# Kernel tuning notes

Hardware: AMD Instinct MI355X
Metric: run time of the kernel (lower is better)

## Reference

```python
import jax, jax.numpy as jnp
import numpy as np

B, S, D, L = 2, 1024, 1024, 48
K = max(1, int(L * 0.1))  # = 4, matches torch k = max(1, int(num_paths * 0.1))
EPS = 1e-5  # torch LayerNorm default


def setup_inputs() -> dict:
    key = jax.random.key(0)
    ks = jax.random.split(key, 7)
    inv = 1.0 / np.sqrt(D).astype(np.float32)
    return {
        "x": jax.random.normal(ks[0], (B, S, D), jnp.float32),
        "gate_w": jax.random.normal(ks[1], (L, D), jnp.float32) * inv,          # gate_proj weight [L,D], no bias
        "lattice_weights": jax.random.normal(ks[2], (L, D, D), jnp.float32) * 0.02,
        "out_w": jax.random.normal(ks[3], (D, D), jnp.float32) * inv,            # out_proj weight [D,D]
        "out_b": jnp.zeros((D,), jnp.float32),
        "ln_g": jnp.ones((D,), jnp.float32),
        "ln_b": jnp.zeros((D,), jnp.float32),
    }


def reference(x, gate_w, lattice_weights, out_w, out_b, ln_g, ln_b):
    # Gate: top-k routing over L lattice paths
    logits = jnp.einsum('bsd,ld->bsl', x, gate_w)                 # [B,S,L]
    top_vals, idx = jax.lax.top_k(logits, K)                      # [B,S,K] each (descending, like torch.topk)
    scores = jax.nn.softmax(top_vals, axis=-1)                    # [B,S,K]

    # Mathematically identical to gathering [B,S,K,D,D] expert matrices and
    # weight-summing, but computed as one dense GEMM over all L experts
    # followed by a cheap gather -- avoids the 32GB intermediate.
    out_all = jnp.einsum('bsd,lde->bsle', x, lattice_weights)     # [B,S,L,D]
    sel = jnp.take_along_axis(out_all, idx[..., None], axis=2)    # [B,S,K,D]
    lattice_out = jnp.einsum('bskd,bsk->bsd', sel, scores)        # [B,S,D]

    y = x + jnp.einsum('bsd,ed->bse', lattice_out, out_w) + out_b # residual + out_proj
    mu = jnp.mean(y, axis=-1, keepdims=True)
    var = jnp.mean((y - mu) ** 2, axis=-1, keepdims=True)
    return ln_g * (y - mu) * jax.lax.rsqrt(var + EPS) + ln_b
```

## Files before the change

### kernel.cpp

```cpp
#include <hip/hip_runtime.h>
#include <stdint.h>

#define TT 2048
#define DD 1024
#define LL 48
#define SENT (LL * 256)

typedef __attribute__((ext_vector_type(8))) short short8;
typedef __attribute__((ext_vector_type(4))) float f32x4;

static __device__ __forceinline__ unsigned int f2bf(float f) {
  union { float f; unsigned int u; } v; v.f = f;
  return (v.u + 0x7FFFu + ((v.u >> 16) & 1u)) >> 16;
}
static __device__ __forceinline__ unsigned int pack2(float a, float b) {
  return f2bf(a) | (f2bf(b) << 16);
}

typedef __attribute__((address_space(1))) const void* as1_t;
typedef __attribute__((address_space(3))) void* as3_t;
static __device__ __forceinline__ void gll16(const void* g, void* s) {
  __builtin_amdgcn_global_load_lds((as1_t)g, (as3_t)s, 16, 0, 0);
}

#define VM_WAIT(n) do { asm volatile("s_waitcnt vmcnt(" #n ")" ::: "memory"); \
                        __builtin_amdgcn_sched_barrier(0); } while (0)
#define LGKM0 do { asm volatile("s_waitcnt lgkmcnt(0)" ::: "memory"); \
                   __builtin_amdgcn_sched_barrier(0); } while (0)
#define BAR do { __builtin_amdgcn_s_barrier(); __builtin_amdgcn_sched_barrier(0); } while (0)

__global__ __launch_bounds__(256) void k_gate(
    const float* __restrict__ x, const float* __restrict__ gw,
    unsigned short* __restrict__ xg, int* __restrict__ counts,
    float* __restrict__ bscore, int* __restrict__ tpos)
{
  __shared__ float xs[8][1024];
  __shared__ float lg[8][48];
  __shared__ int tp_s[32];
  const int tid = threadIdx.x;
  const int t0 = blockIdx.x * 8;
  for (int u = tid; u < 2048; u += 256) {
    int tok = u >> 8;
    int c = (u & 255) << 2;
    float4 v = *(const float4*)(x + (size_t)(t0 + tok) * DD + c);
    *(float4*)&xs[tok][c] = v;
  }
  __syncthreads();
  const int lane = tid & 63, wid = tid >> 6;
  for (int li = 0; li < 12; ++li) {
    const int l = wid + (li << 2);
    const float4* gp = (const float4*)(gw + (size_t)l * DD);
    float4 g0 = gp[lane], g1 = gp[lane + 64], g2 = gp[lane + 128], g3 = gp[lane + 192];
    for (int tok = 0; tok < 8; ++tok) {
      const float4* xp = (const float4*)&xs[tok][0];
      float4 a0 = xp[lane], a1 = xp[lane + 64], a2 = xp[lane + 128], a3 = xp[lane + 192];
      float s = a0.x*g0.x + a0.y*g0.y + a0.z*g0.z + a0.w*g0.w
              + a1.x*g1.x + a1.y*g1.y + a1.z*g1.z + a1.w*g1.w
              + a2.x*g2.x + a2.y*g2.y + a2.z*g2.z + a2.w*g2.w
              + a3.x*g3.x + a3.y*g3.y + a3.z*g3.z + a3.w*g3.w;
      #pragma unroll
      for (int off = 32; off; off >>= 1) s += __shfl_down(s, off);
      if (lane == 0) lg[tok][l] = s;
    }
  }
  __syncthreads();
  if (tid < 8) {
    const int tok = tid;
    float v[4]; int id[4];
    unsigned long long taken = 0ull;
    for (int k = 0; k < 4; ++k) {
      float best = -3.4e38f; int bi = 0;
      for (int l = 0; l < 48; ++l) {
        float cand = lg[tok][l];
        if (!((taken >> l) & 1ull) && cand > best) { best = cand; bi = l; }
      }
      taken |= (1ull << bi); v[k] = best; id[k] = bi;
    }
    float e1 = expf(v[1] - v[0]);
    float e2 = expf(v[2] - v[0]);
    float e3 = expf(v[3] - v[0]);
    float inv = 1.0f / (1.0f + e1 + e2 + e3);
    float sc[4] = { inv, e1*inv, e2*inv, e3*inv };
    for (int k = 0; k < 4; ++k) {
      int pos = atomicAdd(&counts[id[k]], 1);
      bscore[id[k] * TT + pos] = sc[k];
      int dst = (pos < 256) ? (id[k] * 256 + pos) : SENT;
      tp_s[tok * 4 + k] = dst;
      tpos[((t0 + tok) << 2) | k] = dst;
    }
  }
  __syncthreads();
  for (int g = 0; g < 32; ++g) {
    int dst = tp_s[g];
    if (dst == SENT) continue;
    const float* src = xs[g >> 2];
    float a0 = src[tid * 4], a1 = src[tid * 4 + 1], a2 = src[tid * 4 + 2], a3 = src[tid * 4 + 3];
    uint2 pk; pk.x = pack2(a0, a1); pk.y = pack2(a2, a3);
    *(uint2*)(xg + (size_t)dst * DD + tid * 4) = pk;
  }
}

__global__ __launch_bounds__(512, 1) void k_expert(
    const unsigned short* __restrict__ xg, const float* __restrict__ W,
    const int* __restrict__ counts, const float* __restrict__ bscore,
    float* __restrict__ selp)
{
  const int l = blockIdx.y;
  const int ncnt = min(counts[l], 256);
  const int n0 = blockIdx.x * 128;
  const int tid = threadIdx.x, lane = tid & 63, wid = tid >> 6;
  const int wr = wid & 3, wc = wid >> 2;
  const int fr = lane & 15, fq = lane >> 4;

  __shared__ alignas(16) unsigned short As[3][256 * 32];
  __shared__ alignas(16) unsigned int   Bs[2][16 * 132];
  __shared__ float scs[256];
  if (tid < 256) scs[tid] = (tid < ncnt) ? bscore[l * TT + tid] : 0.f;

  const unsigned short* asrc0 = xg + ((size_t)l << 18) + (size_t)(tid >> 2) * DD + (tid & 3) * 8;
  const unsigned short* asrc1 = asrc0 + (size_t)128 * DD;
  const int bp = tid >> 5, e0 = (tid & 31) << 2;
  const float* wsrc0 = W + (size_t)l * DD * DD + (size_t)(bp << 1) * DD + n0 + e0;
  const float* wsrc1 = wsrc0 + DD;

  f32x4 acc[4][4];
  #pragma unroll
  for (int m = 0; m < 4; ++m)
    #pragma unroll
    for (int n = 0; n < 4; ++n)
      #pragma unroll
      for (int j = 0; j < 4; ++j) acc[m][n][j] = 0.f;

  float4 rw0[3], rw1[3];

#define E_BLOAD(s, k0) do { \
    rw0[s] = *(const float4*)(wsrc0 + (size_t)(k0) * DD); \
    rw1[s] = *(const float4*)(wsrc1 + (size_t)(k0) * DD); } while (0)
#define E_ASTAGE(buf, k0) do { \
    gll16(asrc0 + (k0), &As[buf][tid * 8]); \
    gll16(asrc1 + (k0), &As[buf][(512 + tid) * 8]); } while (0)
#define E_BSTORE(buf, s) do { \
    uint4 pv; \
    pv.x = pack2(rw0[s].x, rw1[s].x); pv.y = pack2(rw0[s].y, rw1[s].y); \
    pv.z = pack2(rw0[s].z, rw1[s].z); pv.w = pack2(rw0[s].w, rw1[s].w); \
    *(uint4*)&Bs[buf][bp * 132 + e0] = pv; } while (0)
#define E_COMPUTE(ab, bb) do { \
    const unsigned short* Ab = As[ab]; const unsigned int* Bb = Bs[bb]; \
    short8 af[4], bf[4]; \
    _Pragma("unroll") for (int m = 0; m < 4; ++m) \
      af[m] = *(const short8*)(Ab + (wr * 64 + m * 16 + fr) * 32 + fq * 8); \
    _Pragma("unroll") for (int n = 0; n < 4; ++n) { \
      const int e = wc * 64 + n * 16 + fr; \
      uint4 q; \
      q.x = Bb[(fq * 4 + 0) * 132 + e]; q.y = Bb[(fq * 4 + 1) * 132 + e]; \
      q.z = Bb[(fq * 4 + 2) * 132 + e]; q.w = Bb[(fq * 4 + 3) * 132 + e]; \
      bf[n] = *(short8*)&q; } \
    _Pragma("unroll") for (int m = 0; m < 4; ++m) \
      _Pragma("unroll") for (int n = 0; n < 4; ++n) \
        acc[m][n] = __builtin_amdgcn_mfma_f32_16x16x32_bf16(af[m], bf[n], acc[m][n], 0, 0, 0); \
  } while (0)

  E_BLOAD(0, 0); E_BLOAD(1, 32); E_BLOAD(2, 64);
  E_ASTAGE(0, 0); E_ASTAGE(1, 32);
  VM_WAIT(8);
  E_BSTORE(0, 0);
  E_BLOAD(0, 96);
  VM_WAIT(4);
  LGKM0; BAR;
  E_ASTAGE(2, 64);
  E_COMPUTE(0, 0);
  E_BSTORE(1, 1);
  #pragma unroll
  for (int t = 1; t <= 28; ++t) {
    E_BLOAD((t + 3) % 3, (t + 3) * 32);
    VM_WAIT(6);
    LGKM0; BAR;
    E_ASTAGE((t + 2) % 3, (t + 2) * 32);
    E_COMPUTE(t % 3, t & 1);
    E_BSTORE((t + 1) & 1, (t + 1) % 3);
  }
  VM_WAIT(4);
  LGKM0; BAR;
  E_ASTAGE(1, 31 * 32);
  E_COMPUTE(2, 1);
  E_BSTORE(0, 0);
  VM_WAIT(0);
  LGKM0; BAR;
  E_COMPUTE(0, 0);
  E_BSTORE(1, 1);
  LGKM0; BAR;
  E_COMPUTE(1, 1);

#undef E_BLOAD
#undef E_ASTAGE
#undef E_BSTORE
#undef E_COMPUTE

  #pragma unroll
  for (int m = 0; m < 4; ++m) {
    #pragma unroll
    for (int j = 0; j < 4; ++j) {
      const int r = wr * 64 + m * 16 + fq * 4 + j;
      if (r < ncnt) {
        const float sc = scs[r];
        float* op = selp + (size_t)(l * 256 + r) * DD + n0 + wc * 64 + fr;
        #pragma unroll
        for (int n = 0; n < 4; ++n) op[n * 16] = acc[m][n][j] * sc;
      }
    }
  }
}

__global__ __launch_bounds__(256) void k_combine(const float* __restrict__ selp,
    const int* __restrict__ tpos, unsigned short* __restrict__ lat)
{
  const size_t i = ((size_t)blockIdx.x * 256 + threadIdx.x) << 2;
  const size_t t = i >> 10, d = i & 1023;
  int4 tp = *(const int4*)(tpos + (t << 2));
  float4 s0 = *(const float4*)(selp + (size_t)tp.x * DD + d);
  float4 s1 = *(const float4*)(selp + (size_t)tp.y * DD + d);
  float4 s2 = *(const float4*)(selp + (size_t)tp.z * DD + d);
  float4 s3 = *(const float4*)(selp + (size_t)tp.w * DD + d);
  float r0 = s0.x + s1.x + s2.x + s3.x;
  float r1 = s0.y + s1.y + s2.y + s3.y;
  float r2 = s0.z + s1.z + s2.z + s3.z;
  float r3 = s0.w + s1.w + s2.w + s3.w;
  uint2 pk; pk.x = pack2(r0, r1); pk.y = pack2(r2, r3);
  *(uint2*)(lat + i) = pk;
}

__global__ __launch_bounds__(256, 2) void k_outproj(
    const unsigned short* __restrict__ lat, const float* __restrict__ W2,
    const float* __restrict__ xres, const float* __restrict__ bias,
    float* __restrict__ y)
{
  const int n0 = blockIdx.x * 64;
  const int m0 = blockIdx.y * 128;
  const int tid = threadIdx.x, lane = tid & 63, wid = tid >> 6;

  __shared__ alignas(16) unsigned short As[2][128][40];
  __shared__ alignas(16) unsigned short Bs[2][64][40];

  const int aq = tid >> 2, aseg = tid & 3;
  const unsigned short* la0 = lat + (size_t)(m0 + aq) * DD + aseg * 8;
  const unsigned short* la1 = lat + (size_t)(m0 + aq + 64) * DD + aseg * 8;
  const int be = tid >> 2, bks = tid & 3;
  const float* wb = W2 + (size_t)(n0 + be) * DD + bks * 8;

  f32x4 acc[2][4];
  #pragma unroll
  for (int m = 0; m < 2; ++m)
    #pragma unroll
    for (int n = 0; n < 4; ++n)
      #pragma unroll
      for (int j = 0; j < 4; ++j) acc[m][n][j] = 0.f;

  int4 av0, av1;
  float4 w0, w1;

#define O_LOAD(kk) do { \
    av0 = *(const int4*)(la0 + (kk)); \
    av1 = *(const int4*)(la1 + (kk)); \
    w0 = *(const float4*)(wb + (kk)); \
    w1 = *(const float4*)(wb + (kk) + 4); \
  } while (0)

#define O_STORE(b) do { \
    *(int4*)&As[b][aq][aseg * 8]      = av0; \
    *(int4*)&As[b][aq + 64][aseg * 8] = av1; \
    uint4 pv; \
    pv.x = pack2(w0.x, w0.y); pv.y = pack2(w0.z, w0.w); \
    pv.z = pack2(w1.x, w1.y); pv.w = pack2(w1.z, w1.w); \
    *(uint4*)&Bs[b][be][bks * 8] = pv; \
  } while (0)

  O_LOAD(0); O_STORE(0); __syncthreads();
  int cur = 0;
  for (int t = 0; t < 32; ++t) {
    const bool more = (t < 31);
    if (more) O_LOAD((t + 1) * 32);
    short8 af[2], bf[4];
    #pragma unroll
    for (int n = 0; n < 4; ++n)
      bf[n] = *(const short8*)&Bs[cur][n * 16 + (lane & 15)][(lane >> 4) * 8];
    #pragma unroll
    for (int m = 0; m < 2; ++m)
      af[m] = *(const short8*)&As[cur][wid * 32 + m * 16 + (lane & 15)][(lane >> 4) * 8];
    #pragma unroll
    for (int m = 0; m < 2; ++m)
      #pragma unroll
      for (int n = 0; n < 4; ++n)
        acc[m][n] = __builtin_amdgcn_mfma_f32_16x16x32_bf16(af[m], bf[n], acc[m][n], 0, 0, 0);
    if (more) O_STORE(cur ^ 1);
    __syncthreads();
    cur ^= 1;
  }
#undef O_LOAD
#undef O_STORE

  #pragma unroll
  for (int m = 0; m < 2; ++m) {
    #pragma unroll
    for (int j = 0; j < 4; ++j) {
      const int t = m0 + wid * 32 + m * 16 + ((lane >> 4) << 2) + j;
      #pragma unroll
      for (int n = 0; n < 4; ++n) {
        const int e = n0 + n * 16 + (lane & 15);
        y[(size_t)t * DD + e] = xres[(size_t)t * DD + e] + acc[m][n][j] + bias[e];
      }
    }
  }
}

__global__ __launch_bounds__(256) void k_ln(const float* __restrict__ y,
    const float* __restrict__ g, const float* __restrict__ b, float* __restrict__ out)
{
  const int t = blockIdx.x, tid = threadIdx.x;
  float4 v = *(const float4*)(y + (size_t)t * DD + tid * 4);
  float s  = v.x + v.y + v.z + v.w;
  float ss = v.x*v.x + v.y*v.y + v.z*v.z + v.w*v.w;
  #pragma unroll
  for (int off = 32; off; off >>= 1) { s += __shfl_down(s, off); ss += __shfl_down(ss, off); }
  __shared__ float rs[8];
  const int wid = tid >> 6, lane = tid & 63;
  if (lane == 0) { rs[wid] = s; rs[wid + 4] = ss; }
  __syncthreads();
  float S  = rs[0] + rs[1] + rs[2] + rs[3];
  float SS = rs[4] + rs[5] + rs[6] + rs[7];
  float mu = S * (1.0f / DD);
  float var = SS * (1.0f / DD) - mu * mu;
  float inv = rsqrtf(var + 1e-5f);
  float4 gg = *(const float4*)(g + tid * 4);
  float4 bb = *(const float4*)(b + tid * 4);
  float4 o;
  o.x = gg.x * (v.x - mu) * inv + bb.x;
  o.y = gg.y * (v.y - mu) * inv + bb.y;
  o.z = gg.z * (v.z - mu) * inv + bb.z;
  o.w = gg.w * (v.w - mu) * inv + bb.w;
  *(float4*)(out + (size_t)t * DD + tid * 4) = o;
}

extern "C" void kernel_launch(void* const* d_in, const int* in_sizes, int n_in,
                              void* d_out, int out_size, void* d_ws, size_t ws_size,
                              hipStream_t stream) {
  (void)in_sizes; (void)n_in; (void)out_size;
  const float* x   = (const float*)d_in[0];
  const float* gw  = (const float*)d_in[1];
  const float* lw  = (const float*)d_in[2];
  const float* ow  = (const float*)d_in[3];
  const float* obv = (const float*)d_in[4];
  const float* lng = (const float*)d_in[5];
  const float* lnb = (const float*)d_in[6];
  float* out = (float*)d_out;
  char* ws = (char*)d_ws;

  unsigned short* xg     = (unsigned short*)(ws);
  float*          selp   = (float*)(ws + (24ull << 20));
  unsigned short* lat    = (unsigned short*)(ws + (73ull << 20));
  float*          y      = (float*)(ws + (77ull << 20));
  int*            counts = (int*)(ws + (85ull << 20));
  float*          bscore = (float*)(ws + (85ull << 20) + 4096);
  int*            tpos   = (int*)(ws + (86ull << 20));
  if (ws_size < (87ull << 20)) return;

  hipMemsetAsync(counts, 0, LL * sizeof(int), stream);
  hipMemsetAsync(selp + (size_t)SENT * DD, 0, DD * sizeof(float), stream);
  k_gate<<<TT / 8, 256, 0, stream>>>(x, gw, xg, counts, bscore, tpos);
  k_expert<<<dim3(8, LL), 512, 0, stream>>>(xg, lw, counts, bscore, selp);
  k_combine<<<TT * DD / (256 * 4), 256, 0, stream>>>(selp, tpos, lat);
  k_outproj<<<dim3(16, 16), 256, 0, stream>>>(lat, ow, x, obv, y);
  k_ln<<<TT, 256, 0, stream>>>(y, lng, lnb, out);
}
```

Measured before the change: 193.2 us.

## Shrink expert tile to 256x64, load A fragments directly into registers

The expert GEMM kernel now uses 256-thread blocks covering 64 output columns, giving 768 blocks instead of 384 and allowing up to 3 blocks per CU. The A-operand (gathered bf16 tokens) is no longer staged through LDS with global_load_lds. Each wave reads its MFMA fragments straight from global memory into a double-buffered register set. Only the converted W tile goes through LDS, and the pipeline is restructured around this. The aim is higher occupancy and less LDS traffic, at the cost of uncoalesced 16-byte A reads and more register pressure. Each token row is also reread by every column block, which doubles A global traffic.

Measured after the change: 191.1 us. About the same (-1.1%).

```diff
diff --git a/kernel.cpp b/kernel.cpp
--- a/kernel.cpp
+++ b/kernel.cpp
@@ -17,14 +17,6 @@
   return f2bf(a) | (f2bf(b) << 16);
 }
 
-typedef __attribute__((address_space(1))) const void* as1_t;
-typedef __attribute__((address_space(3))) void* as3_t;
-static __device__ __forceinline__ void gll16(const void* g, void* s) {
-  __builtin_amdgcn_global_load_lds((as1_t)g, (as3_t)s, 16, 0, 0);
-}
-
-#define VM_WAIT(n) do { asm volatile("s_waitcnt vmcnt(" #n ")" ::: "memory"); \
-                        __builtin_amdgcn_sched_barrier(0); } while (0)
 #define LGKM0 do { asm volatile("s_waitcnt lgkmcnt(0)" ::: "memory"); \
                    __builtin_amdgcn_sched_barrier(0); } while (0)
 #define BAR do { __builtin_amdgcn_s_barrier(); __builtin_amdgcn_sched_barrier(0); } while (0)
@@ -100,26 +92,26 @@
   }
 }
 
-__global__ __launch_bounds__(512, 1) void k_expert(
+__global__ __launch_bounds__(256, 3) void k_expert(
     const unsigned short* __restrict__ xg, const float* __restrict__ W,
     const int* __restrict__ counts, const float* __restrict__ bscore,
     float* __restrict__ selp)
 {
   const int l = blockIdx.y;
   const int ncnt = min(counts[l], 256);
-  const int n0 = blockIdx.x * 128;
-  const int tid = threadIdx.x, lane = tid & 63, wid = tid >> 6;
-  const int wr = wid & 3, wc = wid >> 2;
+  const int n0 = blockIdx.x * 64;
+  const int tid = threadIdx.x, lane = tid & 63, wr = tid >> 6;
   const int fr = lane & 15, fq = lane >> 4;
 
-  __shared__ alignas(16) unsigned short As[3][256 * 32];
-  __shared__ alignas(16) unsigned int   Bs[2][16 * 132];
+  __shared__ alignas(16) unsigned int Bs[2][16 * 66];
   __shared__ float scs[256];
-  if (tid < 256) scs[tid] = (tid < ncnt) ? bscore[l * TT + tid] : 0.f;
-
-  const unsigned short* asrc0 = xg + ((size_t)l << 18) + (size_t)(tid >> 2) * DD + (tid & 3) * 8;
-  const unsigned short* asrc1 = asrc0 + (size_t)128 * DD;
-  const int bp = tid >> 5, e0 = (tid & 31) << 2;
+  scs[tid] = (tid < ncnt) ? bscore[l * TT + tid] : 0.f;
+
+  const unsigned short* ap[4];
+  #pragma unroll
+  for (int m = 0; m < 4; ++m)
+    ap[m] = xg + ((size_t)l << 18) + (size_t)(wr * 64 + m * 16 + fr) * DD + fq * 8;
+  const int bp = tid >> 4, e0 = (tid & 15) << 2;
   const float* wsrc0 = W + (size_t)l * DD * DD + (size_t)(bp << 1) * DD + n0 + e0;
   const float* wsrc1 = wsrc0 + DD;
 
@@ -131,70 +123,69 @@
       #pragma unroll
       for (int j = 0; j < 4; ++j) acc[m][n][j] = 0.f;
 
-  float4 rw0[3], rw1[3];
+  short8 af[2][4];
+  float4 rw0[4], rw1[4];
 
 #define E_BLOAD(s, k0) do { \
     rw0[s] = *(const float4*)(wsrc0 + (size_t)(k0) * DD); \
     rw1[s] = *(const float4*)(wsrc1 + (size_t)(k0) * DD); } while (0)
-#define E_ASTAGE(buf, k0) do { \
-    gll16(asrc0 + (k0), &As[buf][tid * 8]); \
-    gll16(asrc1 + (k0), &As[buf][(512 + tid) * 8]); } while (0)
+#define E_ALOAD(p, k0) do { \
+    af[p][0] = *(const short8*)(ap[0] + (k0)); \
+    af[p][1] = *(const short8*)(ap[1] + (k0)); \
+    af[p][2] = *(const short8*)(ap[2] + (k0)); \
+    af[p][3] = *(const short8*)(ap[3] + (k0)); } while (0)
 #define E_BSTORE(buf, s) do { \
     uint4 pv; \
     pv.x = pack2(rw0[s].x, rw1[s].x); pv.y = pack2(rw0[s].y, rw1[s].y); \
     pv.z = pack2(rw0[s].z, rw1[s].z); pv.w = pack2(rw0[s].w, rw1[s].w); \
-    *(uint4*)&Bs[buf][bp * 132 + e0] = pv; } while (0)
-#define E_COMPUTE(ab, bb) do { \
-    const unsigned short* Ab = As[ab]; const unsigned int* Bb = Bs[bb]; \
-    short8 af[4], bf[4]; \
-    _Pragma("unroll") for (int m = 0; m < 4; ++m) \
-      af[m] = *(const short8*)(Ab + (wr * 64 + m * 16 + fr) * 32 + fq * 8); \
+    *(uint4*)&Bs[buf][bp * 66 + e0] = pv; } while (0)
+#define E_COMPUTE(p) do { \
+    const unsigned int* Bb = Bs[p]; \
+    short8 bf[4]; \
     _Pragma("unroll") for (int n = 0; n < 4; ++n) { \
-      const int e = wc * 64 + n * 16 + fr; \
+      const int e = n * 16 + fr; \
       uint4 q; \
-      q.x = Bb[(fq * 4 + 0) * 132 + e]; q.y = Bb[(fq * 4 + 1) * 132 + e]; \
-      q.z = Bb[(fq * 4 + 2) * 132 + e]; q.w = Bb[(fq * 4 + 3) * 132 + e]; \
+      q.x = Bb[(fq * 4 + 0) * 66 + e]; q.y = Bb[(fq * 4 + 1) * 66 + e]; \
+      q.z = Bb[(fq * 4 + 2) * 66 + e]; q.w = Bb[(fq * 4 + 3) * 66 + e]; \
       bf[n] = *(short8*)&q; } \
     _Pragma("unroll") for (int m = 0; m < 4; ++m) \
       _Pragma("unroll") for (int n = 0; n < 4; ++n) \
-        acc[m][n] = __builtin_amdgcn_mfma_f32_16x16x32_bf16(af[m], bf[n], acc[m][n], 0, 0, 0); \
+        acc[m][n] = __builtin_amdgcn_mfma_f32_16x16x32_bf16(af[p][m], bf[n], acc[m][n], 0, 0, 0); \
   } while (0)
 
+#define E_BODY(P, PA, SL, SS, T) do { \
+    E_BLOAD(SL, (T + 3) * 32); \
+    E_ALOAD(PA, (T + 1) * 32); \
+    LGKM0; BAR; \
+    E_BSTORE(PA, SS); \
+    E_COMPUTE(P); } while (0)
+
   E_BLOAD(0, 0); E_BLOAD(1, 32); E_BLOAD(2, 64);
-  E_ASTAGE(0, 0); E_ASTAGE(1, 32);
-  VM_WAIT(8);
+  E_ALOAD(0, 0);
   E_BSTORE(0, 0);
-  E_BLOAD(0, 96);
-  VM_WAIT(4);
+  for (int t = 0; t < 28; t += 4) {
+    E_BODY(0, 1, 3, 1, t + 0);
+    E_BODY(1, 0, 0, 2, t + 1);
+    E_BODY(0, 1, 1, 3, t + 2);
+    E_BODY(1, 0, 2, 0, t + 3);
+  }
+  E_BODY(0, 1, 3, 1, 28);
+  E_ALOAD(0, 30 * 32);
   LGKM0; BAR;
-  E_ASTAGE(2, 64);
-  E_COMPUTE(0, 0);
-  E_BSTORE(1, 1);
-  #pragma unroll
-  for (int t = 1; t <= 28; ++t) {
-    E_BLOAD((t + 3) % 3, (t + 3) * 32);
-    VM_WAIT(6);
-    LGKM0; BAR;
-    E_ASTAGE((t + 2) % 3, (t + 2) * 32);
-    E_COMPUTE(t % 3, t & 1);
-    E_BSTORE((t + 1) & 1, (t + 1) % 3);
-  }
-  VM_WAIT(4);
+  E_BSTORE(0, 2);
+  E_COMPUTE(1);
+  E_ALOAD(1, 31 * 32);
   LGKM0; BAR;
-  E_ASTAGE(1, 31 * 32);
-  E_COMPUTE(2, 1);
-  E_BSTORE(0, 0);
-  VM_WAIT(0);
+  E_BSTORE(1, 3);
+  E_COMPUTE(0);
   LGKM0; BAR;
-  E_COMPUTE(0, 0);
-  E_BSTORE(1, 1);
-  LGKM0; BAR;
-  E_COMPUTE(1, 1);
+  E_COMPUTE(1);
 
 #undef E_BLOAD
-#undef E_ASTAGE
+#undef E_ALOAD
 #undef E_BSTORE
 #undef E_COMPUTE
+#undef E_BODY
 
   #pragma unroll
   for (int m = 0; m < 4; ++m) {
@@ -203,7 +194,7 @@
       const int r = wr * 64 + m * 16 + fq * 4 + j;
       if (r < ncnt) {
         const float sc = scs[r];
-        float* op = selp + (size_t)(l * 256 + r) * DD + n0 + wc * 64 + fr;
+        float* op = selp + (size_t)(l * 256 + r) * DD + n0 + fr;
         #pragma unroll
         for (int n = 0; n < 4; ++n) op[n * 16] = acc[m][n][j] * sc;
       }
@@ -366,7 +357,7 @@
   hipMemsetAsync(counts, 0, LL * sizeof(int), stream);
   hipMemsetAsync(selp + (size_t)SENT * DD, 0, DD * sizeof(float), stream);
   k_gate<<<TT / 8, 256, 0, stream>>>(x, gw, xg, counts, bscore, tpos);
-  k_expert<<<dim3(8, LL), 512, 0, stream>>>(xg, lw, counts, bscore, selp);
+  k_expert<<<dim3(16, LL), 256, 0, stream>>>(xg, lw, counts, bscore, selp);
   k_combine<<<TT * DD / (256 * 4), 256, 0, stream>>>(selp, tpos, lat);
   k_outproj<<<dim3(16, 16), 256, 0, stream>>>(lat, ow, x, obv, y);
   k_ln<<<TT, 256, 0, stream>>>(y, lng, lnb, out);
```

## Pre-convert expert weights to swizzled bf16 and retile expert GEMM

Applied to the files above, without the earlier changes.

Adds a kernel that converts the fp32 expert weights into transposed, XOR-swizzled bf16 each call. The expert GEMM can then stage both A and B straight into LDS with global_load_lds. The GEMM is retiled to 256x256 output tiles with a K step of 64, double buffering and a flat 192-block grid, and gate now writes xg in the matching swizzled layout. This removes the in-register fp32-to-bf16 packing and the bank-conflicted B reads from the GEMM main loop. In exchange it adds an extra pass that reads 192MB of fp32 and writes 96MB of bf16 per call, and needs a larger workspace.

Result: slower. 249.3 us (+29.0%).

```diff
diff --git a/kernel.cpp b/kernel.cpp
--- a/kernel.cpp
+++ b/kernel.cpp
@@ -23,11 +23,11 @@
   __builtin_amdgcn_global_load_lds((as1_t)g, (as3_t)s, 16, 0, 0);
 }
 
-#define VM_WAIT(n) do { asm volatile("s_waitcnt vmcnt(" #n ")" ::: "memory"); \
-                        __builtin_amdgcn_sched_barrier(0); } while (0)
 #define LGKM0 do { asm volatile("s_waitcnt lgkmcnt(0)" ::: "memory"); \
                    __builtin_amdgcn_sched_barrier(0); } while (0)
-#define BAR do { __builtin_amdgcn_s_barrier(); __builtin_amdgcn_sched_barrier(0); } while (0)
+#define VM0   do { asm volatile("s_waitcnt vmcnt(0)" ::: "memory"); \
+                   __builtin_amdgcn_sched_barrier(0); } while (0)
+#define BAR   do { __builtin_amdgcn_s_barrier(); __builtin_amdgcn_sched_barrier(0); } while (0)
 
 __global__ __launch_bounds__(256) void k_gate(
     const float* __restrict__ x, const float* __restrict__ gw,
@@ -90,122 +90,153 @@
     }
   }
   __syncthreads();
-  for (int g = 0; g < 32; ++g) {
-    int dst = tp_s[g];
-    if (dst == SENT) continue;
-    const float* src = xs[g >> 2];
-    float a0 = src[tid * 4], a1 = src[tid * 4 + 1], a2 = src[tid * 4 + 2], a3 = src[tid * 4 + 3];
-    uint2 pk; pk.x = pack2(a0, a1); pk.y = pack2(a2, a3);
-    *(uint2*)(xg + (size_t)dst * DD + tid * 4) = pk;
+  {
+    const int c = tid >> 4, v = (tid >> 1) & 7, h = tid & 1;
+    for (int g = 0; g < 32; ++g) {
+      int dst = tp_s[g];
+      if (dst == SENT) continue;
+      const float* src = xs[g >> 2];
+      float a0 = src[tid*4], a1 = src[tid*4+1], a2 = src[tid*4+2], a3 = src[tid*4+3];
+      uint2 pk; pk.x = pack2(a0, a1); pk.y = pack2(a2, a3);
+      const int p = v ^ (dst & 7);
+      *(uint2*)(xg + (size_t)dst * DD + c * 64 + p * 8 + h * 4) = pk;
+    }
+  }
+}
+
+__global__ __launch_bounds__(256) void k_wconv(const float* __restrict__ W,
+                                               unsigned short* __restrict__ Wt)
+{
+  const int l = blockIdx.z, d0 = blockIdx.y * 128, e0 = blockIdx.x * 128;
+  __shared__ unsigned short T[128][136];
+  const float* src = W + (size_t)l * DD * DD;
+  const int tid = threadIdx.x;
+  #pragma unroll
+  for (int i = 0; i < 16; ++i) {
+    int fl = i * 256 + tid;
+    int d = fl >> 5, e4 = fl & 31;
+    float4 v = *(const float4*)(src + (size_t)(d0 + d) * DD + e0 + e4 * 4);
+    #pragma unroll
+    for (int j = 0; j < 4; ++j) {
+      int e = e4 * 4 + j;
+      int unit = (d >> 3) ^ (e & 7);
+      float fv = (j == 0) ? v.x : (j == 1) ? v.y : (j == 2) ? v.z : v.w;
+      T[e][unit * 8 + (d & 7)] = (unsigned short)f2bf(fv);
+    }
+  }
+  __syncthreads();
+  #pragma unroll
+  for (int i2 = 0; i2 < 8; ++i2) {
+    int uo = i2 * 256 + tid;
+    int e = uo >> 4, ds = uo & 15;
+    short8 s8 = *(const short8*)&T[e][(ds ^ (e & 7)) * 8];
+    int od = d0 + (ds >> 3) * 64 + (((ds & 7) ^ (e & 7)) * 8);
+    *(short8*)(Wt + ((size_t)l << 20) + (size_t)(e0 + e) * DD + od) = s8;
   }
 }
 
 __global__ __launch_bounds__(512, 1) void k_expert(
-    const unsigned short* __restrict__ xg, const float* __restrict__ W,
+    const unsigned short* __restrict__ xg, const unsigned short* __restrict__ Wt,
     const int* __restrict__ counts, const float* __restrict__ bscore,
     float* __restrict__ selp)
 {
-  const int l = blockIdx.y;
+  const int bid = blockIdx.x;
+  const int l = bid % LL;
+  const int n0 = (bid / LL) * 256;
   const int ncnt = min(counts[l], 256);
-  const int n0 = blockIdx.x * 128;
   const int tid = threadIdx.x, lane = tid & 63, wid = tid >> 6;
-  const int wr = wid & 3, wc = wid >> 2;
+  const int mh = wid & 1, nq = wid >> 1;
   const int fr = lane & 15, fq = lane >> 4;
 
-  __shared__ alignas(16) unsigned short As[3][256 * 32];
-  __shared__ alignas(16) unsigned int   Bs[2][16 * 132];
+  __shared__ unsigned short As[2][256][64];
+  __shared__ unsigned short Bs[2][256][64];
   __shared__ float scs[256];
   if (tid < 256) scs[tid] = (tid < ncnt) ? bscore[l * TT + tid] : 0.f;
 
-  const unsigned short* asrc0 = xg + ((size_t)l << 18) + (size_t)(tid >> 2) * DD + (tid & 3) * 8;
-  const unsigned short* asrc1 = asrc0 + (size_t)128 * DD;
-  const int bp = tid >> 5, e0 = (tid & 31) << 2;
-  const float* wsrc0 = W + (size_t)l * DD * DD + (size_t)(bp << 1) * DD + n0 + e0;
-  const float* wsrc1 = wsrc0 + DD;
-
-  f32x4 acc[4][4];
-  #pragma unroll
-  for (int m = 0; m < 4; ++m)
+  const int srow = tid >> 3, sp = tid & 7;
+  const unsigned short* ax = xg + ((size_t)l << 18) + sp * 8;
+  const unsigned short* bx = Wt + ((size_t)l << 20) + (size_t)n0 * DD + sp * 8;
+  size_t soff[4]; int loff[4];
+  #pragma unroll
+  for (int i = 0; i < 4; ++i) {
+    const int row = i * 64 + srow;
+    soff[i] = (size_t)row * DD;
+    loff[i] = row * 64 + sp * 8;
+  }
+
+  const int sw0 = ((fq ^ (fr & 7)) << 3);
+  const int sw1 = sw0 ^ 32;
+
+  f32x4 acc[8][4];
+  #pragma unroll
+  for (int m = 0; m < 8; ++m)
     #pragma unroll
     for (int n = 0; n < 4; ++n)
       #pragma unroll
       for (int j = 0; j < 4; ++j) acc[m][n][j] = 0.f;
 
-  float4 rw0[3], rw1[3];
-
-#define E_BLOAD(s, k0) do { \
-    rw0[s] = *(const float4*)(wsrc0 + (size_t)(k0) * DD); \
-    rw1[s] = *(const float4*)(wsrc1 + (size_t)(k0) * DD); } while (0)
-#define E_ASTAGE(buf, k0) do { \
-    gll16(asrc0 + (k0), &As[buf][tid * 8]); \
-    gll16(asrc1 + (k0), &As[buf][(512 + tid) * 8]); } while (0)
-#define E_BSTORE(buf, s) do { \
-    uint4 pv; \
-    pv.x = pack2(rw0[s].x, rw1[s].x); pv.y = pack2(rw0[s].y, rw1[s].y); \
-    pv.z = pack2(rw0[s].z, rw1[s].z); pv.w = pack2(rw0[s].w, rw1[s].w); \
-    *(uint4*)&Bs[buf][bp * 132 + e0] = pv; } while (0)
-#define E_COMPUTE(ab, bb) do { \
-    const unsigned short* Ab = As[ab]; const unsigned int* Bb = Bs[bb]; \
-    short8 af[4], bf[4]; \
-    _Pragma("unroll") for (int m = 0; m < 4; ++m) \
-      af[m] = *(const short8*)(Ab + (wr * 64 + m * 16 + fr) * 32 + fq * 8); \
+  short8 bf[4];
+
+#define STG_A(i, nb, tc) gll16(ax + soff[i] + (tc) * 64, (unsigned short*)&As[nb][0][0] + loff[i])
+#define STG_B(i, nb, tc) gll16(bx + soff[i] + (tc) * 64, (unsigned short*)&Bs[nb][0][0] + loff[i])
+
+#define RDB(bb, sw) do { \
+    _Pragma("unroll") for (int n = 0; n < 4; ++n) \
+      bf[n] = *(const short8*)&Bs[bb][nq * 64 + n * 16 + fr][sw]; } while (0)
+
+#define PHASE(bb, sw, mg, EXTRA) do { \
+    short8 a0 = *(const short8*)&As[bb][mh * 128 + ((mg)*4+0) * 16 + fr][sw]; \
+    short8 a1 = *(const short8*)&As[bb][mh * 128 + ((mg)*4+1) * 16 + fr][sw]; \
+    short8 a2 = *(const short8*)&As[bb][mh * 128 + ((mg)*4+2) * 16 + fr][sw]; \
+    short8 a3 = *(const short8*)&As[bb][mh * 128 + ((mg)*4+3) * 16 + fr][sw]; \
+    EXTRA; \
+    LGKM0; \
+    __builtin_amdgcn_s_setprio(1); \
     _Pragma("unroll") for (int n = 0; n < 4; ++n) { \
-      const int e = wc * 64 + n * 16 + fr; \
-      uint4 q; \
-      q.x = Bb[(fq * 4 + 0) * 132 + e]; q.y = Bb[(fq * 4 + 1) * 132 + e]; \
-      q.z = Bb[(fq * 4 + 2) * 132 + e]; q.w = Bb[(fq * 4 + 3) * 132 + e]; \
-      bf[n] = *(short8*)&q; } \
-    _Pragma("unroll") for (int m = 0; m < 4; ++m) \
-      _Pragma("unroll") for (int n = 0; n < 4; ++n) \
-        acc[m][n] = __builtin_amdgcn_mfma_f32_16x16x32_bf16(af[m], bf[n], acc[m][n], 0, 0, 0); \
+      acc[(mg)*4+0][n] = __builtin_amdgcn_mfma_f32_16x16x32_bf16(a0, bf[n], acc[(mg)*4+0][n], 0, 0, 0); \
+      acc[(mg)*4+1][n] = __builtin_amdgcn_mfma_f32_16x16x32_bf16(a1, bf[n], acc[(mg)*4+1][n], 0, 0, 0); \
+      acc[(mg)*4+2][n] = __builtin_amdgcn_mfma_f32_16x16x32_bf16(a2, bf[n], acc[(mg)*4+2][n], 0, 0, 0); \
+      acc[(mg)*4+3][n] = __builtin_amdgcn_mfma_f32_16x16x32_bf16(a3, bf[n], acc[(mg)*4+3][n], 0, 0, 0); \
+    } \
+    __builtin_amdgcn_s_setprio(0); \
   } while (0)
 
-  E_BLOAD(0, 0); E_BLOAD(1, 32); E_BLOAD(2, 64);
-  E_ASTAGE(0, 0); E_ASTAGE(1, 32);
-  VM_WAIT(8);
-  E_BSTORE(0, 0);
-  E_BLOAD(0, 96);
-  VM_WAIT(4);
-  LGKM0; BAR;
-  E_ASTAGE(2, 64);
-  E_COMPUTE(0, 0);
-  E_BSTORE(1, 1);
-  #pragma unroll
-  for (int t = 1; t <= 28; ++t) {
-    E_BLOAD((t + 3) % 3, (t + 3) * 32);
-    VM_WAIT(6);
-    LGKM0; BAR;
-    E_ASTAGE((t + 2) % 3, (t + 2) * 32);
-    E_COMPUTE(t % 3, t & 1);
-    E_BSTORE((t + 1) & 1, (t + 1) % 3);
-  }
-  VM_WAIT(4);
-  LGKM0; BAR;
-  E_ASTAGE(1, 31 * 32);
-  E_COMPUTE(2, 1);
-  E_BSTORE(0, 0);
-  VM_WAIT(0);
-  LGKM0; BAR;
-  E_COMPUTE(0, 0);
-  E_BSTORE(1, 1);
-  LGKM0; BAR;
-  E_COMPUTE(1, 1);
-
-#undef E_BLOAD
-#undef E_ASTAGE
-#undef E_BSTORE
-#undef E_COMPUTE
-
-  #pragma unroll
-  for (int m = 0; m < 4; ++m) {
+  #pragma unroll
+  for (int i = 0; i < 4; ++i) STG_A(i, 0, 0);
+  #pragma unroll
+  for (int i = 0; i < 4; ++i) STG_B(i, 0, 0);
+  VM0; BAR;
+
+  int b = 0;
+  for (int t = 0; t < 16; ++t) {
+    const int nb = b ^ 1, tc = t + 1;
+    const bool pre = (t < 15);
+    RDB(b, sw0);
+    PHASE(b, sw0, 0, { if (pre) { STG_A(0, nb, tc); STG_A(1, nb, tc); } });
+    PHASE(b, sw0, 1, { if (pre) { STG_A(2, nb, tc); STG_A(3, nb, tc); } });
+    RDB(b, sw1);
+    PHASE(b, sw1, 0, { if (pre) { STG_B(0, nb, tc); STG_B(1, nb, tc); } });
+    PHASE(b, sw1, 1, { if (pre) { STG_B(2, nb, tc); STG_B(3, nb, tc); } });
+    if (pre) { VM0; }
+    BAR;
+    b = nb;
+  }
+
+#undef STG_A
+#undef STG_B
+#undef RDB
+#undef PHASE
+
+  #pragma unroll
+  for (int mf = 0; mf < 8; ++mf) {
     #pragma unroll
     for (int j = 0; j < 4; ++j) {
-      const int r = wr * 64 + m * 16 + fq * 4 + j;
+      const int r = mh * 128 + mf * 16 + fq * 4 + j;
       if (r < ncnt) {
         const float sc = scs[r];
-        float* op = selp + (size_t)(l * 256 + r) * DD + n0 + wc * 64 + fr;
+        float* op = selp + (size_t)(l * 256 + r) * DD + n0 + nq * 64 + fr;
         #pragma unroll
-        for (int n = 0; n < 4; ++n) op[n * 16] = acc[m][n][j] * sc;
+        for (int n = 0; n < 4; ++n) op[n * 16] = acc[mf][n][j] * sc;
       }
     }
   }
@@ -361,12 +392,14 @@
   int*            counts = (int*)(ws + (85ull << 20));
   float*          bscore = (float*)(ws + (85ull << 20) + 4096);
   int*            tpos   = (int*)(ws + (86ull << 20));
-  if (ws_size < (87ull << 20)) return;
+  unsigned short* Wt     = (unsigned short*)(ws + (96ull << 20));
+  if (ws_size < (193ull << 20)) return;
 
   hipMemsetAsync(counts, 0, LL * sizeof(int), stream);
   hipMemsetAsync(selp + (size_t)SENT * DD, 0, DD * sizeof(float), stream);
   k_gate<<<TT / 8, 256, 0, stream>>>(x, gw, xg, counts, bscore, tpos);
-  k_expert<<<dim3(8, LL), 512, 0, stream>>>(xg, lw, counts, bscore, selp);
+  k_wconv<<<dim3(8, 8, LL), 256, 0, stream>>>(lw, Wt);
+  k_expert<<<192, 512, 0, stream>>>(xg, Wt, counts, bscore, selp);
   k_combine<<<TT * DD / (256 * 4), 256, 0, stream>>>(selp, tpos, lat);
   k_outproj<<<dim3(16, 16), 256, 0, stream>>>(lat, ow, x, obv, y);
   k_ln<<<TT, 256, 0, stream>>>(y, lng, lnb, out);
```

## Retile expert GEMM into smaller 128x64 blocks with occupancy and empty-tile skipping

Applied to the files above, without the earlier changes.

The expert GEMM moves from 384 blocks of 512 threads, each computing a 256x128 tile, to 1536 blocks of 256 threads, each computing a 128x64 tile. Blocks whose 128-row half has no routed tokens exit early. The A tile in LDS uses an XOR swizzle, and the pipeline is reduced to double buffering. The aim is more waves per CU, better latency hiding, and skipping work for lightly loaded experts. In exchange, W columns are reloaded by both row-half blocks, so global traffic on the fp32 weights goes up.

Measured after the change: 186.1 us. 1.04x faster.

```diff
diff --git a/kernel.cpp b/kernel.cpp
--- a/kernel.cpp
+++ b/kernel.cpp
@@ -23,11 +23,9 @@
   __builtin_amdgcn_global_load_lds((as1_t)g, (as3_t)s, 16, 0, 0);
 }
 
-#define VM_WAIT(n) do { asm volatile("s_waitcnt vmcnt(" #n ")" ::: "memory"); \
-                        __builtin_amdgcn_sched_barrier(0); } while (0)
 #define LGKM0 do { asm volatile("s_waitcnt lgkmcnt(0)" ::: "memory"); \
                    __builtin_amdgcn_sched_barrier(0); } while (0)
-#define BAR do { __builtin_amdgcn_s_barrier(); __builtin_amdgcn_sched_barrier(0); } while (0)
+#define BARR  do { __builtin_amdgcn_s_barrier(); __builtin_amdgcn_sched_barrier(0); } while (0)
 
 __global__ __launch_bounds__(256) void k_gate(
     const float* __restrict__ x, const float* __restrict__ gw,
@@ -100,112 +98,121 @@
   }
 }
 
-__global__ __launch_bounds__(512, 1) void k_expert(
+__global__ __launch_bounds__(256, 4) void k_expert(
     const unsigned short* __restrict__ xg, const float* __restrict__ W,
     const int* __restrict__ counts, const float* __restrict__ bscore,
     float* __restrict__ selp)
 {
-  const int l = blockIdx.y;
+  const int bid = blockIdx.x;
+  const int l = bid % LL;
+  const int tcode = bid / LL;
+  const int mh = tcode & 1;
+  const int n0 = (tcode >> 1) * 64;
   const int ncnt = min(counts[l], 256);
-  const int n0 = blockIdx.x * 128;
+  if (mh * 128 >= ncnt) return;
   const int tid = threadIdx.x, lane = tid & 63, wid = tid >> 6;
-  const int wr = wid & 3, wc = wid >> 2;
+  const int mw = wid >> 1, nw = wid & 1;
   const int fr = lane & 15, fq = lane >> 4;
 
-  __shared__ alignas(16) unsigned short As[3][256 * 32];
-  __shared__ alignas(16) unsigned int   Bs[2][16 * 132];
-  __shared__ float scs[256];
-  if (tid < 256) scs[tid] = (tid < ncnt) ? bscore[l * TT + tid] : 0.f;
-
-  const unsigned short* asrc0 = xg + ((size_t)l << 18) + (size_t)(tid >> 2) * DD + (tid & 3) * 8;
-  const unsigned short* asrc1 = asrc0 + (size_t)128 * DD;
-  const int bp = tid >> 5, e0 = (tid & 31) << 2;
-  const float* wsrc0 = W + (size_t)l * DD * DD + (size_t)(bp << 1) * DD + n0 + e0;
+  __shared__ unsigned short As[2][128][32];
+  __shared__ unsigned int   Bs[2][16 * 68];
+
+  const int arow = tid >> 2;
+  const int aslot = (tid & 3) ^ ((tid >> 2) & 3);
+  const unsigned short* ax0 = xg + ((size_t)(l * 256 + mh * 128 + arow) << 10) + aslot * 8;
+  const unsigned short* ax1 = ax0 + ((size_t)64 << 10);
+  const int bp = tid >> 4, be = (tid & 15) << 2;
+  const float* wsrc0 = W + (size_t)l * DD * DD + (size_t)(bp << 1) * DD + n0 + be;
   const float* wsrc1 = wsrc0 + DD;
 
-  f32x4 acc[4][4];
+  const int asw = (fq ^ (fr & 3)) * 8;
+  int aoff[4];
+  #pragma unroll
+  for (int mf = 0; mf < 4; ++mf)
+    aoff[mf] = (mw * 64 + mf * 16 + fr) * 32 + asw;
+  const int ebase = nw * 32 + fr;
+
+  f32x4 acc[4][2];
   #pragma unroll
   for (int m = 0; m < 4; ++m)
     #pragma unroll
-    for (int n = 0; n < 4; ++n)
+    for (int n = 0; n < 2; ++n)
       #pragma unroll
       for (int j = 0; j < 4; ++j) acc[m][n][j] = 0.f;
 
-  float4 rw0[3], rw1[3];
-
-#define E_BLOAD(s, k0) do { \
-    rw0[s] = *(const float4*)(wsrc0 + (size_t)(k0) * DD); \
-    rw1[s] = *(const float4*)(wsrc1 + (size_t)(k0) * DD); } while (0)
-#define E_ASTAGE(buf, k0) do { \
-    gll16(asrc0 + (k0), &As[buf][tid * 8]); \
-    gll16(asrc1 + (k0), &As[buf][(512 + tid) * 8]); } while (0)
-#define E_BSTORE(buf, s) do { \
+  float4 ga[2], gb[2];
+
+#define G_LD(S, T) do { \
+    ga[S] = *(const float4*)(wsrc0 + (size_t)(T) * 32 * DD); \
+    gb[S] = *(const float4*)(wsrc1 + (size_t)(T) * 32 * DD); } while (0)
+#define S_A(BF, T) do { \
+    gll16(ax0 + (T) * 32, &As[BF][arow][(tid & 3) * 8]); \
+    gll16(ax1 + (T) * 32, &As[BF][arow + 64][(tid & 3) * 8]); } while (0)
+#define B_ST(BF, S) do { \
     uint4 pv; \
-    pv.x = pack2(rw0[s].x, rw1[s].x); pv.y = pack2(rw0[s].y, rw1[s].y); \
-    pv.z = pack2(rw0[s].z, rw1[s].z); pv.w = pack2(rw0[s].w, rw1[s].w); \
-    *(uint4*)&Bs[buf][bp * 132 + e0] = pv; } while (0)
-#define E_COMPUTE(ab, bb) do { \
-    const unsigned short* Ab = As[ab]; const unsigned int* Bb = Bs[bb]; \
-    short8 af[4], bf[4]; \
-    _Pragma("unroll") for (int m = 0; m < 4; ++m) \
-      af[m] = *(const short8*)(Ab + (wr * 64 + m * 16 + fr) * 32 + fq * 8); \
-    _Pragma("unroll") for (int n = 0; n < 4; ++n) { \
-      const int e = wc * 64 + n * 16 + fr; \
+    pv.x = pack2(ga[S].x, gb[S].x); pv.y = pack2(ga[S].y, gb[S].y); \
+    pv.z = pack2(ga[S].z, gb[S].z); pv.w = pack2(ga[S].w, gb[S].w); \
+    *(uint4*)&Bs[BF][bp * 68 + be] = pv; } while (0)
+#define CMP(BF) do { \
+    const unsigned int* Bb = Bs[BF]; \
+    short8 bf[2]; \
+    _Pragma("unroll") for (int n = 0; n < 2; ++n) { \
       uint4 q; \
-      q.x = Bb[(fq * 4 + 0) * 132 + e]; q.y = Bb[(fq * 4 + 1) * 132 + e]; \
-      q.z = Bb[(fq * 4 + 2) * 132 + e]; q.w = Bb[(fq * 4 + 3) * 132 + e]; \
+      q.x = Bb[(fq * 4 + 0) * 68 + ebase + n * 16]; \
+      q.y = Bb[(fq * 4 + 1) * 68 + ebase + n * 16]; \
+      q.z = Bb[(fq * 4 + 2) * 68 + ebase + n * 16]; \
+      q.w = Bb[(fq * 4 + 3) * 68 + ebase + n * 16]; \
       bf[n] = *(short8*)&q; } \
-    _Pragma("unroll") for (int m = 0; m < 4; ++m) \
-      _Pragma("unroll") for (int n = 0; n < 4; ++n) \
-        acc[m][n] = __builtin_amdgcn_mfma_f32_16x16x32_bf16(af[m], bf[n], acc[m][n], 0, 0, 0); \
+    _Pragma("unroll") for (int mf = 0; mf < 4; ++mf) { \
+      short8 af = *(const short8*)((const unsigned short*)As[BF] + aoff[mf]); \
+      acc[mf][0] = __builtin_amdgcn_mfma_f32_16x16x32_bf16(af, bf[0], acc[mf][0], 0, 0, 0); \
+      acc[mf][1] = __builtin_amdgcn_mfma_f32_16x16x32_bf16(af, bf[1], acc[mf][1], 0, 0, 0); } \
   } while (0)
 
-  E_BLOAD(0, 0); E_BLOAD(1, 32); E_BLOAD(2, 64);
-  E_ASTAGE(0, 0); E_ASTAGE(1, 32);
-  VM_WAIT(8);
-  E_BSTORE(0, 0);
-  E_BLOAD(0, 96);
-  VM_WAIT(4);
-  LGKM0; BAR;
-  E_ASTAGE(2, 64);
-  E_COMPUTE(0, 0);
-  E_BSTORE(1, 1);
-  #pragma unroll
-  for (int t = 1; t <= 28; ++t) {
-    E_BLOAD((t + 3) % 3, (t + 3) * 32);
-    VM_WAIT(6);
-    LGKM0; BAR;
-    E_ASTAGE((t + 2) % 3, (t + 2) * 32);
-    E_COMPUTE(t % 3, t & 1);
-    E_BSTORE((t + 1) & 1, (t + 1) % 3);
-  }
-  VM_WAIT(4);
-  LGKM0; BAR;
-  E_ASTAGE(1, 31 * 32);
-  E_COMPUTE(2, 1);
-  E_BSTORE(0, 0);
-  VM_WAIT(0);
-  LGKM0; BAR;
-  E_COMPUTE(0, 0);
-  E_BSTORE(1, 1);
-  LGKM0; BAR;
-  E_COMPUTE(1, 1);
-
-#undef E_BLOAD
-#undef E_ASTAGE
-#undef E_BSTORE
-#undef E_COMPUTE
-
-  #pragma unroll
-  for (int m = 0; m < 4; ++m) {
+#define VMW(N) do { asm volatile("s_waitcnt vmcnt(" #N ")" ::: "memory"); \
+                    __builtin_amdgcn_sched_barrier(0); } while (0)
+
+#define E_IT(P, T) do { \
+    G_LD(P, (T) + 2);                 \
+    VMW(2);                           \
+    LGKM0; BARR;                      \
+    S_A(P ^ 1, (T) + 1); \
+    B_ST(P ^ 1, P ^ 1); \
+    CMP(P); \
+  } while (0)
+
+  G_LD(0, 0); G_LD(1, 1);
+  S_A(0, 0);
+  VMW(4);
+  B_ST(0, 0);
+  for (int t = 0; t < 30; t += 2) {
+    E_IT(0, t);
+    E_IT(1, t + 1);
+  }
+  VMW(0); LGKM0; BARR;
+  S_A(1, 31);
+  B_ST(1, 1);
+  CMP(0);
+  VMW(0); LGKM0; BARR;
+  CMP(1);
+
+#undef G_LD
+#undef S_A
+#undef B_ST
+#undef CMP
+#undef VMW
+#undef E_IT
+
+  #pragma unroll
+  for (int mf = 0; mf < 4; ++mf) {
     #pragma unroll
     for (int j = 0; j < 4; ++j) {
-      const int r = wr * 64 + m * 16 + fq * 4 + j;
+      const int r = mh * 128 + mw * 64 + mf * 16 + fq * 4 + j;
       if (r < ncnt) {
-        const float sc = scs[r];
-        float* op = selp + (size_t)(l * 256 + r) * DD + n0 + wc * 64 + fr;
-        #pragma unroll
-        for (int n = 0; n < 4; ++n) op[n * 16] = acc[m][n][j] * sc;
+        const float sc = bscore[l * TT + r];
+        float* op = selp + ((size_t)(l * 256 + r) << 10) + n0 + nw * 32 + fr;
+        op[0]  = acc[mf][0][j] * sc;
+        op[16] = acc[mf][1][j] * sc;
       }
     }
   }
@@ -366,7 +373,7 @@
   hipMemsetAsync(counts, 0, LL * sizeof(int), stream);
   hipMemsetAsync(selp + (size_t)SENT * DD, 0, DD * sizeof(float), stream);
   k_gate<<<TT / 8, 256, 0, stream>>>(x, gw, xg, counts, bscore, tpos);
-  k_expert<<<dim3(8, LL), 512, 0, stream>>>(xg, lw, counts, bscore, selp);
+  k_expert<<<1536, 256, 0, stream>>>(xg, lw, counts, bscore, selp);
   k_combine<<<TT * DD / (256 * 4), 256, 0, stream>>>(selp, tpos, lat);
   k_outproj<<<dim3(16, 16), 256, 0, stream>>>(lat, ow, x, obv, y);
   k_ln<<<TT, 256, 0, stream>>>(y, lng, lnb, out);
```
